# Kernel optimization log

Measured on AMD Instinct MI355X. Metric: run time of the kernel, lower is better.

## Reference

```python
import jax, jax.numpy as jnp
import numpy as np

N, D, T = 4096, 256, 32
GAMMA = 1.0 / 256.0  # 1/d
ALPHA = 1.0


def _rbf_kernel(X, Y, gamma):
    # K[i, j] = exp(-gamma * ||X[i] - Y[j]||^2), vectorized (replaces the
    # original per-(i,j) Python double loop).
    x2 = jnp.sum(X * X, axis=1)  # [n]
    y2 = jnp.sum(Y * Y, axis=1)  # [m]
    d2 = x2[:, None] + y2[None, :] - 2.0 * (X @ Y.T)  # [n, m]
    d2 = jnp.maximum(d2, 0.0)  # numerical guard; exact form is non-negative
    return jnp.exp(-gamma * d2)


def setup_inputs() -> dict:
    key = jax.random.key(0)
    kx, ky = jax.random.split(key)
    X = jax.random.normal(kx, (N, D), dtype=jnp.float32)
    y = jax.random.normal(ky, (N, T), dtype=jnp.float32)
    return {"X": X, "y": y}


def reference(X, y):
    # fit: K = rbf(X, X); dual = solve(K + alpha*I, y)
    K = _rbf_kernel(X, X, GAMMA)  # [N, N]
    A = K + ALPHA * jnp.eye(N, dtype=K.dtype)
    dual_coef = jnp.linalg.solve(A, y)  # [N, T]
    # predict(X): original recomputes rbf(X, X) == K, then K @ dual_coef
    y_pred = K @ dual_coef  # [N, T]
    return y_pred
```

## Files before the change

### kernel.cpp

```cpp
#include <hip/hip_runtime.h>
#include <math.h>

#define NN 4096
#define DD 256
#define TT 32
#define GAMMA (1.0f/256.0f)
#define ITERS 10
#define JBP 8
#define JCH 512
#define IB  128
#define BROW (JCH + 8)
#define KC  64
#define KBP 72

typedef __attribute__((ext_vector_type(8))) _Float16 f16x8;
typedef __attribute__((ext_vector_type(4))) _Float16 f16x4;
typedef __attribute__((ext_vector_type(4))) float f32x4;

__global__ __launch_bounds__(256) void setup(const float* __restrict__ X,
                                             float* __restrict__ x2,
                                             _Float16* __restrict__ Xh,
                                             const float* __restrict__ y,
                                             float* __restrict__ r,
                                             _Float16* __restrict__ vh,
                                             _Float16* __restrict__ vl,
                                             float* __restrict__ rrp) {
    const int b = blockIdx.x, tid = threadIdx.x;
    const int wid = tid >> 6, lane = tid & 63;
    if (b < 1024) {
        int row = b * 4 + wid;
        const float* xr = X + (size_t)row * DD;
        float4 v = *(const float4*)(xr + lane * 4);
        float s = v.x * v.x + v.y * v.y + v.z * v.z + v.w * v.w;
        #pragma unroll
        for (int o = 32; o; o >>= 1) s += __shfl_down(s, o);
        if (lane == 0) x2[row] = s;
        f16x4 h;
        h[0] = (_Float16)v.x; h[1] = (_Float16)v.y; h[2] = (_Float16)v.z; h[3] = (_Float16)v.w;
        *(f16x4*)(Xh + (size_t)row * DD + lane * 4) = h;
    } else {
        int bb = b - 1024;
        int t = bb >> 3, c = bb & 7;
        float s = 0.f;
        #pragma unroll
        for (int pass = 0; pass < 2; ++pass) {
            int i = c * 512 + pass * 256 + tid;
            float v = y[(size_t)i * TT + t];
            size_t off = (size_t)t * NN + i;
            r[off] = v;
            _Float16 h = (_Float16)v;
            vh[off] = h; vl[off] = (_Float16)(v - (float)h);
            s += v * v;
        }
        #pragma unroll
        for (int o = 32; o; o >>= 1) s += __shfl_down(s, o);
        __shared__ float red[4];
        if (lane == 0) red[wid] = s;
        __syncthreads();
        if (tid == 0) rrp[t * 8 + c] = red[0] + red[1] + red[2] + red[3];
    }
}

__global__ __launch_bounds__(256) void k_build(const _Float16* __restrict__ Xh,
                                               const float* __restrict__ x2,
                                               _Float16* __restrict__ Kh) {
    __shared__ _Float16 As[128 * KBP];
    __shared__ _Float16 Bs[256 * KBP];
    const int i0 = blockIdx.x * 128, j0 = blockIdx.y * 256;
    const int tid = threadIdx.x;
    const int wid = tid >> 6, lane = tid & 63;
    const int wr = wid >> 1, wc = wid & 1;
    const int l15 = lane & 15, l4 = lane >> 4;
    f32x4 acc[4][8] = {};
    for (int kc = 0; kc < DD; kc += KC) {
        __syncthreads();
        #pragma unroll
        for (int s = 0; s < 4; ++s) {
            int idx = s * 256 + tid;
            int row = idx >> 3, c = idx & 7;
            *(uint4*)(As + row * KBP + c * 8) =
                *(const uint4*)(Xh + (size_t)(i0 + row) * DD + kc + c * 8);
        }
        #pragma unroll
        for (int s = 0; s < 8; ++s) {
            int idx = s * 256 + tid;
            int row = idx >> 3, c = idx & 7;
            *(uint4*)(Bs + row * KBP + c * 8) =
                *(const uint4*)(Xh + (size_t)(j0 + row) * DD + kc + c * 8);
        }
        __syncthreads();
        #pragma unroll
        for (int kk = 0; kk < 2; ++kk) {
            f16x8 af[4], bfr[8];
            #pragma unroll
            for (int m = 0; m < 4; ++m)
                af[m] = *(const f16x8*)(As + (wr * 64 + m * 16 + l15) * KBP + kk * 32 + l4 * 8);
            #pragma unroll
            for (int n = 0; n < 8; ++n)
                bfr[n] = *(const f16x8*)(Bs + (wc * 128 + n * 16 + l15) * KBP + kk * 32 + l4 * 8);
            #pragma unroll
            for (int m = 0; m < 4; ++m)
                #pragma unroll
                for (int n = 0; n < 8; ++n)
                    acc[m][n] = __builtin_amdgcn_mfma_f32_16x16x32_f16(af[m], bfr[n], acc[m][n], 0, 0, 0);
        }
    }
    #pragma unroll
    for (int m = 0; m < 4; ++m) {
        #pragma unroll
        for (int rg = 0; rg < 4; ++rg) {
            int i = i0 + wr * 64 + m * 16 + l4 * 4 + rg;
            float x2i = x2[i];
            #pragma unroll
            for (int n = 0; n < 8; ++n) {
                int j = j0 + wc * 128 + n * 16 + l15;
                float d2 = fmaxf(x2i + x2[j] - 2.f * acc[m][n][rg], 0.f);
                Kh[(size_t)i * NN + j] = (_Float16)__expf(-GAMMA * d2);
            }
        }
    }
}

__global__ __launch_bounds__(512) void matvec_part(const _Float16* __restrict__ Kh,
                                                   const _Float16* __restrict__ vh,
                                                   const _Float16* __restrict__ vl,
                                                   const float* __restrict__ r,
                                                   float* __restrict__ part,
                                                   float* __restrict__ rKvp) {
    __shared__ __align__(16) _Float16 Bbuf[2 * 32 * BROW];
    __shared__ float redb[8][33];
    _Float16* Bh = Bbuf;
    _Float16* Bl = Bbuf + 32 * BROW;
    const int ib = blockIdx.x;
    const int jb = blockIdx.y;
    const int bid = jb * 32 + ib;
    const int tid = threadIdx.x;
    const int wid = tid >> 6, lane = tid & 63;
    const int l15 = lane & 15, l4 = lane >> 4;
    #pragma unroll
    for (int s = 0; s < 4; ++s) {
        int c = s * 512 + tid;
        int row = c >> 6, col8 = c & 63;
        *(uint4*)(Bh + row * BROW + col8 * 8) =
            *(const uint4*)(vh + (size_t)row * NN + jb * JCH + col8 * 8);
        *(uint4*)(Bl + row * BROW + col8 * 8) =
            *(const uint4*)(vl + (size_t)row * NN + jb * JCH + col8 * 8);
    }
    __syncthreads();
    const _Float16* Ap  = Kh + (size_t)(ib * IB + wid * 16 + l15) * NN + jb * JCH + l4 * 8;
    const _Float16* bhp = Bh + l15 * BROW + l4 * 8;
    const _Float16* blp = Bl + l15 * BROW + l4 * 8;
    f32x4 acc0 = {}, acc1 = {};
    #pragma unroll 4
    for (int jc = 0; jc < JCH; jc += 32) {
        f16x8 a   = *(const f16x8*)(Ap + jc);
        f16x8 bh0 = *(const f16x8*)(bhp + jc);
        f16x8 bh1 = *(const f16x8*)(bhp + 16 * BROW + jc);
        f16x8 bl0 = *(const f16x8*)(blp + jc);
        f16x8 bl1 = *(const f16x8*)(blp + 16 * BROW + jc);
        acc0 = __builtin_amdgcn_mfma_f32_16x16x32_f16(a, bh0, acc0, 0, 0, 0);
        acc1 = __builtin_amdgcn_mfma_f32_16x16x32_f16(a, bh1, acc1, 0, 0, 0);
        acc0 = __builtin_amdgcn_mfma_f32_16x16x32_f16(a, bl0, acc0, 0, 0, 0);
        acc1 = __builtin_amdgcn_mfma_f32_16x16x32_f16(a, bl1, acc1, 0, 0, 0);
    }
    __syncthreads();
    float* tl = (float*)Bbuf;
    #pragma unroll
    for (int rg = 0; rg < 4; ++rg) {
        tl[(wid * 32 + l15) * 17 + l4 * 4 + rg]      = acc0[rg];
        tl[(wid * 32 + 16 + l15) * 17 + l4 * 4 + rg] = acc1[rg];
    }
    __syncthreads();
    #pragma unroll
    for (int q = 0; q < 8; ++q) {
        int idx = q * 64 + lane;
        int t = idx >> 4, il = idx & 15;
        int gi = ib * IB + wid * 16 + il;
        float val = tl[(wid * 32 + t) * 17 + il];
        part[((size_t)jb * TT + t) * NN + gi] = val;
        float cq = r[(size_t)t * NN + gi] * val;
        #pragma unroll
        for (int o = 8; o; o >>= 1) cq += __shfl_down(cq, o);
        if (il == 0) redb[wid][t] = cq;
    }
    __syncthreads();
    if (tid < 32) {
        float s = 0.f;
        #pragma unroll
        for (int u = 0; u < 8; ++u) s += redb[u][tid];
        rKvp[tid * 256 + bid] = s;
    }
}

__global__ __launch_bounds__(512) void cupd(const float* __restrict__ part, float* __restrict__ r,
                                            float* __restrict__ p, float* __restrict__ s_,
                                            float* __restrict__ x, float* __restrict__ ax,
                                            _Float16* __restrict__ vh,
                                            _Float16* __restrict__ vl,
                                            const float* __restrict__ rrp_in,
                                            float* __restrict__ rrp_out,
                                            const float* __restrict__ rKvp,
                                            const float* __restrict__ scal_in,
                                            float* __restrict__ scal_out,
                                            float* __restrict__ out,
                                            int first, int last) {
    const int t = blockIdx.x, c = blockIdx.y, tid = threadIdx.x;
    const int wid = tid >> 6, lane = tid & 63;
    __shared__ float sc2[2];
    __shared__ float red[8];
    if (wid == 0) {
        float rw_ = 0.f;
        #pragma unroll
        for (int u = 0; u < 4; ++u) rw_ += rKvp[t * 256 + u * 64 + lane];
        float rr_ = (lane < 8) ? rrp_in[t * 8 + lane] : 0.f;
        #pragma unroll
        for (int o = 32; o; o >>= 1) { rw_ += __shfl_down(rw_, o); rr_ += __shfl_down(rr_, o); }
        if (lane == 0) {
            float rr = rr_;
            float rw = rw_ + rr;
            float alpha, beta;
            if (first) { beta = 0.f; alpha = rr / rw; }
            else {
                float ap = scal_in[t], rrprev = scal_in[TT + t];
                beta = rr / rrprev;
                alpha = rr / (rw - (beta / ap) * rr);
            }
            sc2[0] = alpha; sc2[1] = beta;
            if (c == 0) { scal_out[t] = alpha; scal_out[TT + t] = rr; }
        }
    }
    __syncthreads();
    const float alpha = sc2[0], beta = sc2[1];
    int i = c * 512 + tid;
    size_t off = (size_t)t * NN + i;
    float s = 0.f;
    #pragma unroll
    for (int b = 0; b < JBP; ++b) s += part[((size_t)b * TT + t) * NN + i];
    float rv = r[off];
    float wv = s + rv;
    float pn = first ? rv : fmaf(beta, p[off], rv);
    float sn = first ? wv : fmaf(beta, s_[off], wv);
    p[off] = pn; s_[off] = sn;
    float xn  = (first ? 0.f : x[off])  + alpha * pn;
    float axn = (first ? 0.f : ax[off]) + alpha * sn;
    x[off] = xn; ax[off] = axn;
    float rn = rv - alpha * sn;
    r[off] = rn;
    if (last) {
        out[(size_t)i * TT + t] = axn - xn;
    } else {
        _Float16 h = (_Float16)rn;
        vh[off] = h; vl[off] = (_Float16)(rn - (float)h);
    }
    float v = rn * rn;
    #pragma unroll
    for (int o = 32; o; o >>= 1) v += __shfl_down(v, o);
    if (lane == 0) red[wid] = v;
    __syncthreads();
    if (tid == 0) {
        float tot = 0.f;
        #pragma unroll
        for (int u = 0; u < 8; ++u) tot += red[u];
        rrp_out[t * 8 + c] = tot;
    }
}

extern "C" void kernel_launch(void* const* d_in, const int* in_sizes, int n_in,
                              void* d_out, int out_size, void* d_ws, size_t ws_size,
                              hipStream_t stream) {
    const float* X = (const float*)d_in[0];
    const float* y = (const float*)d_in[1];
    float* out = (float*)d_out;

    unsigned char* wsb = (unsigned char*)d_ws;
    _Float16* Kh = (_Float16*)wsb;  wsb += (size_t)NN * NN * 2;
    float* part  = (float*)wsb;     wsb += (size_t)JBP * TT * NN * 4;
    float* r     = (float*)wsb;     wsb += (size_t)TT * NN * 4;
    float* p     = (float*)wsb;     wsb += (size_t)TT * NN * 4;
    float* s_    = (float*)wsb;     wsb += (size_t)TT * NN * 4;
    float* x     = (float*)wsb;     wsb += (size_t)TT * NN * 4;
    float* ax    = (float*)wsb;     wsb += (size_t)TT * NN * 4;
    _Float16* vh = (_Float16*)wsb;  wsb += (size_t)TT * NN * 2;
    _Float16* vl = (_Float16*)wsb;  wsb += (size_t)TT * NN * 2;
    _Float16* Xh = (_Float16*)wsb;  wsb += (size_t)NN * DD * 2;
    float* x2v   = (float*)wsb;     wsb += (size_t)NN * 4;
    float* rrp   = (float*)wsb;     wsb += 512 * 4;
    float* rKvp  = (float*)wsb;     wsb += (size_t)TT * 256 * 4;
    float* scal  = (float*)wsb;     wsb += 128 * 4;

    setup<<<1280, 256, 0, stream>>>(X, x2v, Xh, y, r, vh, vl, rrp);
    k_build<<<dim3(NN / 128, NN / 256), 256, 0, stream>>>(Xh, x2v, Kh);

    for (int j = 0; j < ITERS; ++j) {
        matvec_part<<<dim3(32, JBP), 512, 0, stream>>>(Kh, vh, vl, r, part, rKvp);
        cupd<<<dim3(TT, 8), 512, 0, stream>>>(part, r, p, s_, x, ax, vh, vl,
                                              rrp + (j & 1) * 256, rrp + ((j + 1) & 1) * 256,
                                              rKvp,
                                              scal + (j & 1) * 64, scal + ((j + 1) & 1) * 64,
                                              out,
                                              j == 0 ? 1 : 0, j == ITERS - 1 ? 1 : 0);
    }
}
```

Measured before the change: 191.8 us.

## Retile k_build to 256x256, halve matvec row block, vectorize CG update

The Gram-matrix build now uses 256x256 output tiles with 512 threads, giving more reuse per loaded X tile and fewer blocks. matvec_part drops to 64-row blocks with 256 threads, doubling the grid to 512 blocks so more CUs are busy on each iteration. The CG update kernel handles two elements per thread with float2 and half2 accesses over a grid cut in half, and the reduction buffer sizes are changed to match. The trade-off is higher register and LDS pressure in k_build and more duplicated B staging per matvec block.

```diff
diff --git a/kernel.cpp b/kernel.cpp
--- a/kernel.cpp
+++ b/kernel.cpp
@@ -8,13 +8,14 @@
 #define ITERS 10
 #define JBP 8
 #define JCH 512
-#define IB  128
+#define IB  64
 #define BROW (JCH + 8)
 #define KC  64
 #define KBP 72
 
 typedef __attribute__((ext_vector_type(8))) _Float16 f16x8;
 typedef __attribute__((ext_vector_type(4))) _Float16 f16x4;
+typedef __attribute__((ext_vector_type(2))) _Float16 f16x2;
 typedef __attribute__((ext_vector_type(4))) float f32x4;
 
 __global__ __launch_bounds__(256) void setup(const float* __restrict__ X,
@@ -40,11 +41,11 @@
         *(f16x4*)(Xh + (size_t)row * DD + lane * 4) = h;
     } else {
         int bb = b - 1024;
-        int t = bb >> 3, c = bb & 7;
+        int t = bb >> 2, c = bb & 3;
         float s = 0.f;
         #pragma unroll
-        for (int pass = 0; pass < 2; ++pass) {
-            int i = c * 512 + pass * 256 + tid;
+        for (int pass = 0; pass < 4; ++pass) {
+            int i = c * 1024 + pass * 256 + tid;
             float v = y[(size_t)i * TT + t];
             size_t off = (size_t)t * NN + i;
             r[off] = v;
@@ -57,33 +58,33 @@
         __shared__ float red[4];
         if (lane == 0) red[wid] = s;
         __syncthreads();
-        if (tid == 0) rrp[t * 8 + c] = red[0] + red[1] + red[2] + red[3];
-    }
-}
-
-__global__ __launch_bounds__(256) void k_build(const _Float16* __restrict__ Xh,
+        if (tid == 0) rrp[t * 4 + c] = red[0] + red[1] + red[2] + red[3];
+    }
+}
+
+__global__ __launch_bounds__(512) void k_build(const _Float16* __restrict__ Xh,
                                                const float* __restrict__ x2,
                                                _Float16* __restrict__ Kh) {
-    __shared__ _Float16 As[128 * KBP];
+    __shared__ _Float16 As[256 * KBP];
     __shared__ _Float16 Bs[256 * KBP];
-    const int i0 = blockIdx.x * 128, j0 = blockIdx.y * 256;
+    const int i0 = blockIdx.x * 256, j0 = blockIdx.y * 256;
     const int tid = threadIdx.x;
     const int wid = tid >> 6, lane = tid & 63;
-    const int wr = wid >> 1, wc = wid & 1;
+    const int wr = wid >> 2, wc = wid & 3;
     const int l15 = lane & 15, l4 = lane >> 4;
-    f32x4 acc[4][8] = {};
+    f32x4 acc[8][4] = {};
     for (int kc = 0; kc < DD; kc += KC) {
         __syncthreads();
         #pragma unroll
         for (int s = 0; s < 4; ++s) {
-            int idx = s * 256 + tid;
+            int idx = s * 512 + tid;
             int row = idx >> 3, c = idx & 7;
             *(uint4*)(As + row * KBP + c * 8) =
                 *(const uint4*)(Xh + (size_t)(i0 + row) * DD + kc + c * 8);
         }
         #pragma unroll
-        for (int s = 0; s < 8; ++s) {
-            int idx = s * 256 + tid;
+        for (int s = 0; s < 4; ++s) {
+            int idx = s * 512 + tid;
             int row = idx >> 3, c = idx & 7;
             *(uint4*)(Bs + row * KBP + c * 8) =
                 *(const uint4*)(Xh + (size_t)(j0 + row) * DD + kc + c * 8);
@@ -91,29 +92,29 @@
         __syncthreads();
         #pragma unroll
         for (int kk = 0; kk < 2; ++kk) {
-            f16x8 af[4], bfr[8];
+            f16x8 af[8], bfr[4];
             #pragma unroll
-            for (int m = 0; m < 4; ++m)
-                af[m] = *(const f16x8*)(As + (wr * 64 + m * 16 + l15) * KBP + kk * 32 + l4 * 8);
+            for (int m = 0; m < 8; ++m)
+                af[m] = *(const f16x8*)(As + (wr * 128 + m * 16 + l15) * KBP + kk * 32 + l4 * 8);
             #pragma unroll
-            for (int n = 0; n < 8; ++n)
-                bfr[n] = *(const f16x8*)(Bs + (wc * 128 + n * 16 + l15) * KBP + kk * 32 + l4 * 8);
+            for (int n = 0; n < 4; ++n)
+                bfr[n] = *(const f16x8*)(Bs + (wc * 64 + n * 16 + l15) * KBP + kk * 32 + l4 * 8);
             #pragma unroll
-            for (int m = 0; m < 4; ++m)
+            for (int m = 0; m < 8; ++m)
                 #pragma unroll
-                for (int n = 0; n < 8; ++n)
+                for (int n = 0; n < 4; ++n)
                     acc[m][n] = __builtin_amdgcn_mfma_f32_16x16x32_f16(af[m], bfr[n], acc[m][n], 0, 0, 0);
         }
     }
     #pragma unroll
-    for (int m = 0; m < 4; ++m) {
+    for (int m = 0; m < 8; ++m) {
         #pragma unroll
         for (int rg = 0; rg < 4; ++rg) {
-            int i = i0 + wr * 64 + m * 16 + l4 * 4 + rg;
+            int i = i0 + wr * 128 + m * 16 + l4 * 4 + rg;
             float x2i = x2[i];
             #pragma unroll
-            for (int n = 0; n < 8; ++n) {
-                int j = j0 + wc * 128 + n * 16 + l15;
+            for (int n = 0; n < 4; ++n) {
+                int j = j0 + wc * 64 + n * 16 + l15;
                 float d2 = fmaxf(x2i + x2[j] - 2.f * acc[m][n][rg], 0.f);
                 Kh[(size_t)i * NN + j] = (_Float16)__expf(-GAMMA * d2);
             }
@@ -121,25 +122,25 @@
     }
 }
 
-__global__ __launch_bounds__(512) void matvec_part(const _Float16* __restrict__ Kh,
+__global__ __launch_bounds__(256) void matvec_part(const _Float16* __restrict__ Kh,
                                                    const _Float16* __restrict__ vh,
                                                    const _Float16* __restrict__ vl,
                                                    const float* __restrict__ r,
                                                    float* __restrict__ part,
                                                    float* __restrict__ rKvp) {
     __shared__ __align__(16) _Float16 Bbuf[2 * 32 * BROW];
-    __shared__ float redb[8][33];
+    __shared__ float redb[4][33];
     _Float16* Bh = Bbuf;
     _Float16* Bl = Bbuf + 32 * BROW;
     const int ib = blockIdx.x;
     const int jb = blockIdx.y;
-    const int bid = jb * 32 + ib;
+    const int bid = jb * 64 + ib;
     const int tid = threadIdx.x;
     const int wid = tid >> 6, lane = tid & 63;
     const int l15 = lane & 15, l4 = lane >> 4;
     #pragma unroll
-    for (int s = 0; s < 4; ++s) {
-        int c = s * 512 + tid;
+    for (int s = 0; s < 8; ++s) {
+        int c = s * 256 + tid;
         int row = c >> 6, col8 = c & 63;
         *(uint4*)(Bh + row * BROW + col8 * 8) =
             *(const uint4*)(vh + (size_t)row * NN + jb * JCH + col8 * 8);
@@ -187,8 +188,8 @@
     if (tid < 32) {
         float s = 0.f;
         #pragma unroll
-        for (int u = 0; u < 8; ++u) s += redb[u][tid];
-        rKvp[tid * 256 + bid] = s;
+        for (int u = 0; u < 4; ++u) s += redb[u][tid];
+        rKvp[tid * 512 + bid] = s;
     }
 }
 
@@ -211,8 +212,8 @@
     if (wid == 0) {
         float rw_ = 0.f;
         #pragma unroll
-        for (int u = 0; u < 4; ++u) rw_ += rKvp[t * 256 + u * 64 + lane];
-        float rr_ = (lane < 8) ? rrp_in[t * 8 + lane] : 0.f;
+        for (int u = 0; u < 8; ++u) rw_ += rKvp[t * 512 + u * 64 + lane];
+        float rr_ = (lane < 4) ? rrp_in[t * 4 + lane] : 0.f;
         #pragma unroll
         for (int o = 32; o; o >>= 1) { rw_ += __shfl_down(rw_, o); rr_ += __shfl_down(rr_, o); }
         if (lane == 0) {
@@ -231,28 +232,45 @@
     }
     __syncthreads();
     const float alpha = sc2[0], beta = sc2[1];
-    int i = c * 512 + tid;
+    int i = c * 1024 + tid * 2;
     size_t off = (size_t)t * NN + i;
-    float s = 0.f;
-    #pragma unroll
-    for (int b = 0; b < JBP; ++b) s += part[((size_t)b * TT + t) * NN + i];
-    float rv = r[off];
-    float wv = s + rv;
-    float pn = first ? rv : fmaf(beta, p[off], rv);
-    float sn = first ? wv : fmaf(beta, s_[off], wv);
-    p[off] = pn; s_[off] = sn;
-    float xn  = (first ? 0.f : x[off])  + alpha * pn;
-    float axn = (first ? 0.f : ax[off]) + alpha * sn;
-    x[off] = xn; ax[off] = axn;
-    float rn = rv - alpha * sn;
-    r[off] = rn;
+    float2 sv = {0.f, 0.f};
+    #pragma unroll
+    for (int b = 0; b < JBP; ++b) {
+        float2 pl = *(const float2*)&part[((size_t)b * TT + t) * NN + i];
+        sv.x += pl.x; sv.y += pl.y;
+    }
+    float2 rv = *(const float2*)(r + off);
+    float2 wv = { sv.x + rv.x, sv.y + rv.y };
+    float2 pv, sv2;
+    if (first) { pv = rv; sv2 = wv; }
+    else {
+        float2 po = *(const float2*)(p + off);
+        float2 so = *(const float2*)(s_ + off);
+        pv  = { fmaf(beta, po.x, rv.x), fmaf(beta, po.y, rv.y) };
+        sv2 = { fmaf(beta, so.x, wv.x), fmaf(beta, so.y, wv.y) };
+    }
+    *(float2*)(p + off) = pv;
+    *(float2*)(s_ + off) = sv2;
+    float2 xo  = first ? float2{0.f, 0.f} : *(const float2*)(x + off);
+    float2 axo = first ? float2{0.f, 0.f} : *(const float2*)(ax + off);
+    float2 xn  = { xo.x + alpha * pv.x,  xo.y + alpha * pv.y };
+    float2 axn = { axo.x + alpha * sv2.x, axo.y + alpha * sv2.y };
+    *(float2*)(x + off) = xn;
+    *(float2*)(ax + off) = axn;
+    float2 rn = { rv.x - alpha * sv2.x, rv.y - alpha * sv2.y };
+    *(float2*)(r + off) = rn;
     if (last) {
-        out[(size_t)i * TT + t] = axn - xn;
+        out[(size_t)i * TT + t]       = axn.x - xn.x;
+        out[(size_t)(i + 1) * TT + t] = axn.y - xn.y;
     } else {
-        _Float16 h = (_Float16)rn;
-        vh[off] = h; vl[off] = (_Float16)(rn - (float)h);
-    }
-    float v = rn * rn;
+        _Float16 h0 = (_Float16)rn.x, h1 = (_Float16)rn.y;
+        f16x2 hv = { h0, h1 };
+        f16x2 lv = { (_Float16)(rn.x - (float)h0), (_Float16)(rn.y - (float)h1) };
+        *(f16x2*)(vh + off) = hv;
+        *(f16x2*)(vl + off) = lv;
+    }
+    float v = rn.x * rn.x + rn.y * rn.y;
     #pragma unroll
     for (int o = 32; o; o >>= 1) v += __shfl_down(v, o);
     if (lane == 0) red[wid] = v;
@@ -261,7 +279,7 @@
         float tot = 0.f;
         #pragma unroll
         for (int u = 0; u < 8; ++u) tot += red[u];
-        rrp_out[t * 8 + c] = tot;
+        rrp_out[t * 4 + c] = tot;
     }
 }
 
@@ -284,17 +302,17 @@
     _Float16* vl = (_Float16*)wsb;  wsb += (size_t)TT * NN * 2;
     _Float16* Xh = (_Float16*)wsb;  wsb += (size_t)NN * DD * 2;
     float* x2v   = (float*)wsb;     wsb += (size_t)NN * 4;
-    float* rrp   = (float*)wsb;     wsb += 512 * 4;
-    float* rKvp  = (float*)wsb;     wsb += (size_t)TT * 256 * 4;
+    float* rrp   = (float*)wsb;     wsb += 256 * 4;
+    float* rKvp  = (float*)wsb;     wsb += (size_t)TT * 512 * 4;
     float* scal  = (float*)wsb;     wsb += 128 * 4;
 
-    setup<<<1280, 256, 0, stream>>>(X, x2v, Xh, y, r, vh, vl, rrp);
-    k_build<<<dim3(NN / 128, NN / 256), 256, 0, stream>>>(Xh, x2v, Kh);
+    setup<<<1152, 256, 0, stream>>>(X, x2v, Xh, y, r, vh, vl, rrp);
+    k_build<<<dim3(NN / 256, NN / 256), 512, 0, stream>>>(Xh, x2v, Kh);
 
     for (int j = 0; j < ITERS; ++j) {
-        matvec_part<<<dim3(32, JBP), 512, 0, stream>>>(Kh, vh, vl, r, part, rKvp);
-        cupd<<<dim3(TT, 8), 512, 0, stream>>>(part, r, p, s_, x, ax, vh, vl,
-                                              rrp + (j & 1) * 256, rrp + ((j + 1) & 1) * 256,
+        matvec_part<<<dim3(64, JBP), 256, 0, stream>>>(Kh, vh, vl, r, part, rKvp);
+        cupd<<<dim3(TT, 4), 512, 0, stream>>>(part, r, p, s_, x, ax, vh, vl,
+                                              rrp + (j & 1) * 128, rrp + ((j + 1) & 1) * 128,
                                               rKvp,
                                               scal + (j & 1) * 64, scal + ((j + 1) & 1) * 64,
                                               out,
```

After: 187.8 us. 1.02x faster.
